# Kernel tuning notes

Measured on AMD Instinct MI355X. Metric: run time of the kernel, lower is better.

Reference implementation:

```python
import jax, jax.numpy as jnp
import numpy as np

EPS = 1e-7
BURN_IN = 3
INNER_STEPS = 2
N_FEAT, N_TARGET, N_LATENT = 262144, 8192, 32


def setup_inputs() -> dict:
    key = jax.random.key(0)
    ks = jax.random.split(key, 8)
    x = jax.random.normal(ks[0], (N_FEAT,), jnp.float32)
    y = jax.random.normal(ks[1], (N_TARGET,), jnp.float32)
    mu_x = jnp.zeros((N_FEAT,), jnp.float32)
    mu_y = jnp.zeros((N_TARGET,), jnp.float32)
    u0 = jax.random.normal(ks[2], (N_LATENT,), jnp.float32)
    u = u0 / jnp.sqrt(jnp.sum(u0 ** 2))
    Wz = jax.random.normal(ks[3], (N_LATENT, N_FEAT), jnp.float32) * 0.1
    Cz = jax.random.normal(ks[4], (N_LATENT, N_TARGET), jnp.float32) * 0.1
    t_sq_sum = jax.random.uniform(ks[5], (N_LATENT,), jnp.float32) + 1.0
    bz = jax.random.normal(ks[6], (N_LATENT,), jnp.float32) * 0.1
    P = jax.random.normal(ks[7], (N_LATENT, N_FEAT), jnp.float32) * 0.1
    return dict(x=x, y=y, mu_x=mu_x, mu_y=mu_y, u=u, Wz=Wz, Cz=Cz,
                t_sq_sum=t_sq_sum, bz=bz, P=P, n=100)


def _partial_fit(x, y, mu_x, mu_y, u, Wz, Cz, t_sq_sum, bz, P, n):
    # n is a static Python int (sample count before this call)
    n_new = n + 1  # torch: self.n[:] = self.n + 1
    mu_x = (mu_x * n_new + x) / (n_new + 1)
    mu_y = (mu_y * n_new + y) / (n_new + 1)
    xc = x - mu_x
    yc = y - mu_y
    if n_new <= BURN_IN:
        # vectorized burn-in update; only Wz and t_sq_sum change
        Wz = Wz + xc[None, :] * u[:, None]
        tz = Wz @ xc / (jnp.sqrt(jnp.sum(Wz ** 2, axis=1)) + EPS)
        t_sq_sum = t_sq_sum + tz * tz
        return mu_x, mu_y, u, Wz, Cz, t_sq_sum, bz, P

    def comp_step(carry, comp):
        xr, yr = carry
        Wz_i, Cz_i, P_i, u_i, tss, bz_i = comp
        # inner power-iteration refinements (total INNER_STEPS passes)
        for _ in range(INNER_STEPS):
            wz = Wz_i + xr * u_i                                  # [n_feat]
            tz = xr @ wz / (jnp.sqrt(jnp.sum(wz ** 2)) + EPS)     # scalar
            tss_ = tss + tz * tz
            t = tz / jnp.sqrt(tss_)
            cz = Cz_i + yr * t                                    # [n_target]
            C_i = cz / jnp.sqrt(jnp.sum(cz ** 2))
            u_i = yr @ C_i
        bz_new = bz_i + u_i * tz
        b = bz_new / jnp.sqrt(tss_)
        P_new = P_i + xr * t
        xr2 = xr - t * P_new  # deflate x
        yr2 = yr - b * t * C_i  # deflate y
        return (xr2, yr2), (wz, cz, P_new, u_i, tss_, bz_new)

    (_, _), (Wz_n, Cz_n, P_n, u_n, tss_n, bz_n) = jax.lax.scan(
        comp_step, (xc, yc), (Wz, Cz, P, u, t_sq_sum, bz))
    return mu_x, mu_y, u_n, Wz_n, Cz_n, tss_n, bz_n, P_n


def reference(x, y, mu_x, mu_y, u, Wz, Cz, t_sq_sum, bz, P, n):
    outs = _partial_fit(x, y, mu_x, mu_y, u, Wz, Cz, t_sq_sum, bz, P, n)
    # concatenate updated state (mu_x, mu_y, u, Wz, Cz, t_sq_sum, bz, P)
    return jnp.concatenate([o.ravel() for o in outs])
```

## Files before the change

kernel.cpp:

```cpp
#include <hip/hip_runtime.h>


#define NF 262144
#define NT 8192
#define NL 32
#define GYS 36
#define LDSW 260

#define NBX 1024
#define KS  256
#define CHK 128
#define NCHK 2
#define NSLOT 128
#define GXW 68
#define PBE 2276
#define DIAG 2244

#define WS_PART 0
#define WS_GY   (NSLOT*PBE)
#define WS_GX   (WS_GY + GYS*GYS)
#define WS_COEF (WS_GX + PBE)

#define OUT_MU_X 0
#define OUT_MU_Y 262144
#define OUT_U    270336
#define OUT_WZ   270368
#define OUT_CZ   8658976
#define OUT_TSS  8921120
#define OUT_BZ   8921152
#define OUT_P    8921184

typedef __attribute__((ext_vector_type(8))) short bf16x8;
typedef __attribute__((ext_vector_type(4))) float f32x4;

__device__ __forceinline__ float4 ld4(const float* p) { return *(const float4*)p; }

__device__ __forceinline__ unsigned int f2bf_rne(float f) {
  unsigned int t = __float_as_uint(f);
  t += 0x7FFFu + ((t >> 16) & 1u);
  return t >> 16;
}

__device__ __forceinline__ double rsq64(double x) {
  double r = __builtin_amdgcn_rsq(x);
  r = r * (1.5 - 0.5 * x * r * r);
  return r;
}

__global__ __launch_bounds__(320) void gram_kernel(
    const float* __restrict__ x, const float* __restrict__ y,
    const float* __restrict__ mux, const float* __restrict__ muy,
    const float* __restrict__ Wz, const float* __restrict__ Cz,
    const float* __restrict__ P, const int* __restrict__ np,
    float* __restrict__ ws)
{
  __shared__ __align__(16) char smem[80 * CHK * 4 + 128];
  const int tid = threadIdx.x;
  const int b = blockIdx.x;
  const float n1 = (float)(np[0] + 1);
  const float cmu = n1 / (n1 + 1.0f);

  if (b < NBX) {
    char* hB = smem;
    char* lB = smem + 80 * CHK * 2;
    float* PB = ws + WS_PART + (size_t)(b & (NSLOT - 1)) * PBE;

    {
      unsigned int* hz = (unsigned int*)hB;
      unsigned int* lz = (unsigned int*)lB;
      for (int i = tid; i < 960; i += 320) { hz[65 * 64 + i] = 0u; lz[65 * 64 + i] = 0u; }
    }

    f32x4 acc0 = {0.f, 0.f, 0.f, 0.f};
    f32x4 acc1 = acc0, acc2 = acc0;
    const int lane = tid & 63;
    const int w = tid >> 6;
    const int col16 = lane & 15;
    const int kgrp = lane >> 4;
    const int swz = (col16 & 7) << 4;

    float4 vA[7], vB[7]; float4 vmA, vmB;

    auto issue = [&](int c, float4* v, float4& vm) {
      const int kb = b * KS + c * CHK;
#pragma unroll
      for (int it = 0; it < 7; ++it) {
        int idx = tid + it * 320;
        if (idx < 2080) {
          int row = idx >> 5;
          int c4 = idx & 31;
          int k = kb + c4 * 4;
          const float* bp = (row == 0) ? (x + k)
                          : (row < 33) ? (P + (size_t)(row - 1) * NF + k)
                                       : (Wz + (size_t)(row - 33) * NF + k);
          v[it] = ld4(bp);
          if (it == 0 && row == 0) vm = ld4(mux + k);
        }
      }
    };

    auto convert_write = [&](float4* v, float4& vm) {
#pragma unroll
      for (int it = 0; it < 7; ++it) {
        int idx = tid + it * 320;
        if (idx < 2080) {
          int row = idx >> 5;
          int c4 = idx & 31;
          float4 t4 = v[it];
          if (it == 0 && row == 0) {
            t4.x = cmu * (t4.x - vm.x); t4.y = cmu * (t4.y - vm.y);
            t4.z = cmu * (t4.z - vm.z); t4.w = cmu * (t4.w - vm.w);
          }
          if (row >= 33) {
            float sq = t4.x * t4.x + t4.y * t4.y + t4.z * t4.z + t4.w * t4.w;
            sq += __shfl_xor(sq, 1, 64);
            sq += __shfl_xor(sq, 2, 64);
            sq += __shfl_xor(sq, 4, 64);
            sq += __shfl_xor(sq, 8, 64);
            sq += __shfl_xor(sq, 16, 64);
            if ((tid & 31) == 0) atomicAdd(&PB[DIAG + row - 33], sq);
          }
          unsigned int b0 = __float_as_uint(t4.x), b1 = __float_as_uint(t4.y);
          unsigned int b2 = __float_as_uint(t4.z), b3 = __float_as_uint(t4.w);
          float h0 = __uint_as_float(b0 & 0xFFFF0000u);
          float h1 = __uint_as_float(b1 & 0xFFFF0000u);
          float h2 = __uint_as_float(b2 & 0xFFFF0000u);
          float h3 = __uint_as_float(b3 & 0xFFFF0000u);
          uint2 hw, lw;
          hw.x = (b0 >> 16) | ((b1 >> 16) << 16);
          hw.y = (b2 >> 16) | ((b3 >> 16) << 16);
          lw.x = f2bf_rne(t4.x - h0) | (f2bf_rne(t4.y - h1) << 16);
          lw.y = f2bf_rne(t4.z - h2) | (f2bf_rne(t4.w - h3) << 16);
          int off = ((row << 8) + (c4 << 3)) ^ ((row & 7) << 4);
          *(uint2*)(hB + off) = hw;
          *(uint2*)(lB + off) = lw;
        }
      }
    };

    auto compute_chunk = [&]() {
#pragma unroll
      for (int s = 0; s < 4; ++s) {
        const int kbyte = s * 64 + kgrp * 16;
        const int oa = ((col16 << 8) + kbyte) ^ swz;
        const int ob = oa + (w << 12);
        bf16x8 bh = *(const bf16x8*)(hB + ob);
        bf16x8 bl = *(const bf16x8*)(lB + ob);
        bf16x8 a0h = *(const bf16x8*)(hB + oa);
        bf16x8 a0l = *(const bf16x8*)(lB + oa);
        acc0 = __builtin_amdgcn_mfma_f32_16x16x32_bf16(a0h, bh, acc0, 0, 0, 0);
        acc0 = __builtin_amdgcn_mfma_f32_16x16x32_bf16(a0h, bl, acc0, 0, 0, 0);
        acc0 = __builtin_amdgcn_mfma_f32_16x16x32_bf16(a0l, bh, acc0, 0, 0, 0);
        acc0 = __builtin_amdgcn_mfma_f32_16x16x32_bf16(a0l, bl, acc0, 0, 0, 0);
        bf16x8 a1h = *(const bf16x8*)(hB + oa + 4096);
        bf16x8 a1l = *(const bf16x8*)(lB + oa + 4096);
        acc1 = __builtin_amdgcn_mfma_f32_16x16x32_bf16(a1h, bh, acc1, 0, 0, 0);
        acc1 = __builtin_amdgcn_mfma_f32_16x16x32_bf16(a1h, bl, acc1, 0, 0, 0);
        acc1 = __builtin_amdgcn_mfma_f32_16x16x32_bf16(a1l, bh, acc1, 0, 0, 0);
        acc1 = __builtin_amdgcn_mfma_f32_16x16x32_bf16(a1l, bl, acc1, 0, 0, 0);
        bf16x8 a2h = *(const bf16x8*)(hB + oa + 8192);
        bf16x8 a2l = *(const bf16x8*)(lB + oa + 8192);
        acc2 = __builtin_amdgcn_mfma_f32_16x16x32_bf16(a2h, bh, acc2, 0, 0, 0);
        acc2 = __builtin_amdgcn_mfma_f32_16x16x32_bf16(a2h, bl, acc2, 0, 0, 0);
        acc2 = __builtin_amdgcn_mfma_f32_16x16x32_bf16(a2l, bh, acc2, 0, 0, 0);
        acc2 = __builtin_amdgcn_mfma_f32_16x16x32_bf16(a2l, bl, acc2, 0, 0, 0);
      }
    };

    issue(0, vA, vmA);
    issue(1, vB, vmB);
    convert_write(vA, vmA);
    __syncthreads();
    compute_chunk();
    __syncthreads();
    convert_write(vB, vmB);
    __syncthreads();
    compute_chunk();

    const int vcol = w * 16 + col16;
    if (vcol < 65) {
#pragma unroll
      for (int r2 = 0; r2 < 4; ++r2) {
        int u = kgrp * 4 + r2;
        atomicAdd(&PB[u * GXW + vcol], acc0[r2]);
        atomicAdd(&PB[(16 + u) * GXW + vcol], acc1[r2]);
      }
      if (kgrp == 0) atomicAdd(&PB[32 * GXW + vcol], acc2[0]);
    }
  } else {
    float* lds = (float*)smem;
    float* GY = ws + WS_GY;
    const int yb = b - NBX;
    int gu = 0, gv = 0; bool active = (tid < 45);
    if (active) {
      int pp = tid;
      for (int g = 0; g < 9; ++g) {
        int cnt = 9 - g;
        if (pp < cnt) { gu = g; gv = g + pp; break; }
        pp -= cnt;
      }
    }
    float acc[16];
#pragma unroll
    for (int i = 0; i < 16; ++i) acc[i] = 0.f;
    const int wb = yb * 256;
    float4 vy[8]; float4 vmy;
#pragma unroll
    for (int it = 0; it < 8; ++it) {
      int idx = tid + it * 320;
      if (idx < 2304) {
        int row = idx >> 6;
        int c4 = idx & 63;
        int k = wb + c4 * 4;
        if (row == 0) {
          vy[it] = ld4(y + k);
          if (it == 0) vmy = ld4(muy + k);
        } else if (row < 33) {
          vy[it] = ld4(Cz + (size_t)(row - 1) * NT + k);
        } else {
          vy[it] = make_float4(0.f, 0.f, 0.f, 0.f);
        }
      }
    }
#pragma unroll
    for (int it = 0; it < 8; ++it) {
      int idx = tid + it * 320;
      if (idx < 2304) {
        int row = idx >> 6;
        int c4 = idx & 63;
        float4 t4 = vy[it];
        if (it == 0 && row == 0) {
          t4.x = cmu * (t4.x - vmy.x); t4.y = cmu * (t4.y - vmy.y);
          t4.z = cmu * (t4.z - vmy.z); t4.w = cmu * (t4.w - vmy.w);
        }
        *(float4*)&lds[row * LDSW + c4 * 4] = t4;
      }
    }
    __syncthreads();
    if (active) {
      const int ub = 4 * gu * LDSW, vb = 4 * gv * LDSW;
      for (int c = 0; c < 64; ++c) {
        float4 av[4], bv[4];
#pragma unroll
        for (int r = 0; r < 4; ++r) av[r] = *(const float4*)&lds[ub + r * LDSW + c * 4];
#pragma unroll
        for (int s = 0; s < 4; ++s) bv[s] = *(const float4*)&lds[vb + s * LDSW + c * 4];
#pragma unroll
        for (int r = 0; r < 4; ++r)
#pragma unroll
          for (int s = 0; s < 4; ++s)
            acc[r * 4 + s] += av[r].x * bv[s].x + av[r].y * bv[s].y +
                              av[r].z * bv[s].z + av[r].w * bv[s].w;
      }
#pragma unroll
      for (int r = 0; r < 4; ++r)
#pragma unroll
        for (int s = 0; s < 4; ++s) {
          int u = 4 * gu + r, v = 4 * gv + s;
          if (u < 33 && v < 33) {
            float val = acc[r * 4 + s];
            atomicAdd(&GY[u * GYS + v], val);
            if (gu != gv) atomicAdd(&GY[v * GYS + u], val);
          }
        }
    }
  }
}

__global__ __launch_bounds__(256) void reduce_kernel(float* __restrict__ ws) {
  const int e = (blockIdx.x % 9) * 256 + threadIdx.x;
  const int c = blockIdx.x / 9;
  if (e < PBE) {
    const float* PB = ws + WS_PART + (size_t)(c * 32) * PBE + e;
    float s0 = 0.f, s1 = 0.f, s2 = 0.f, s3 = 0.f;
#pragma unroll
    for (int j = 0; j < 32; j += 4) {
      s0 += PB[(size_t)j * PBE];
      s1 += PB[(size_t)(j + 1) * PBE];
      s2 += PB[(size_t)(j + 2) * PBE];
      s3 += PB[(size_t)(j + 3) * PBE];
    }
    atomicAdd(ws + WS_GX + e, (s0 + s1) + (s2 + s3));
  }
}

__global__ void solve_kernel(const float* __restrict__ ws,
                             const float* __restrict__ u_in,
                             const float* __restrict__ tss_in,
                             const float* __restrict__ bz_in,
                             float* __restrict__ coef,
                             float* __restrict__ out)
{
  const int l = threadIdx.x;
  const float* GX = ws + WS_GX;
  const float* GY = ws + WS_GY;
  float* AWZT = coef;
  float* APT  = coef + 33 * NL;
  float* ACZT = coef + 66 * NL;

  float rP[32], rW[32], rC[32];
#pragma unroll
  for (int i = 0; i < 32; ++i) rP[i] = GX[(1 + i) * GXW + 1 + l];
#pragma unroll
  for (int i = 0; i < 32; ++i) rW[i] = (l < 32) ? GX[(1 + i) * GXW + 33 + l] : 0.f;
#pragma unroll
  for (int i = 0; i < 32; ++i) rC[i] = GY[(1 + i) * GYS + 1 + l];
  float dS  = (l < 32) ? GX[DIAG + l] : 0.f;
  float u0l = (l < 32) ? u_in[l]   : 0.f;
  float t0l = (l < 32) ? tss_in[l] : 0.f;
  float b0l = (l < 32) ? bz_in[l]  : 0.f;

  double q = (double)GX[0];
  double r = (double)GY[0];
  double pj = (l < 32) ? (double)GX[1 + l]  : 0.0;
  double wj = (l < 32) ? (double)GX[33 + l] : 0.0;
  double ej = (l < 32) ? (double)GY[1 + l]  : 0.0;
  double cx = (l == 0) ? 1.0 : 0.0;
  double cy = (l == 0) ? 1.0 : 0.0;

#pragma unroll
  for (int i = 0; i < NL; ++i) {
    double a  = __shfl(wj, i, 64);
    double g  = __shfl(ej, i, 64);
    double pi = __shfl(pj, i, 64);
    double s  = (double)__shfl(dS, i, 64);
    double h  = (double)__shfl(rC[i], i, 64);
    double Pd = (double)__shfl(rP[i], i, 64);
    double u0   = (double)__shfl(u0l, i, 64);
    double tss0 = (double)__shfl(t0l, i, 64);
    double bz0  = (double)__shfl(b0l, i, 64);

    double ui = u0, u1 = 0.0, tz = 0.0, tss_ = 0.0, t = 0.0;
    double rt = 0.0, rn = 0.0;
#pragma unroll
    for (int pass = 0; pass < 2; ++pass) {
      double num = a + ui * q;
      double s2  = s + 2.0 * ui * a + ui * ui * q;
      double rs  = rsq64(s2);
      tz = num * rs * (1.0 - 1e-7 * rs);
      tss_ = tss0 + tz * tz;
      rt = rsq64(tss_);
      t  = tz * rt;
      double ncz2 = h + 2.0 * t * g + t * t * r;
      rn = rsq64(ncz2);
      ui = (g + t * r) * rn;
      if (pass == 0) u1 = ui;
    }
    double u2 = ui;
    double bz_new = bz0 + u2 * tz;
    double bb = bz_new * rt;
    double phi = 1.0 - t * t;
    double gam = bb * t * rn;
    double psi = 1.0 - gam * t;

    if (l == 0) {
      out[OUT_U + i]   = (float)u2;
      out[OUT_TSS + i] = (float)tss_;
      out[OUT_BZ + i]  = (float)bz_new;
    }
    if (l < 33) {
      AWZT[l * 32 + i] = (float)(u1 * cx);
      APT [l * 32 + i] = (float)(t  * cx) + ((l == 1 + i) ? 1.0f : 0.0f);
      ACZT[l * 32 + i] = (float)(t  * cy) + ((l == 1 + i) ? 1.0f : 0.0f);
    }
    q = phi * phi * q - 2.0 * phi * t * pi + t * t * Pd;
    r = psi * psi * r - 2.0 * psi * gam * g + gam * gam * h;
    cx *= phi; if (l == 1 + i) cx -= t;
    cy *= psi; if (l == 1 + i) cy -= gam;
    if (l < 32) {
      pj = phi * pj - t * (double)rP[i];
      wj = phi * wj - t * (double)rW[i];
      ej = psi * ej - gam * (double)rC[i];
    }
  }
}

__global__ __launch_bounds__(256) void out_kernel(
    const float* __restrict__ x, const float* __restrict__ y,
    const float* __restrict__ mux, const float* __restrict__ muy,
    const float* __restrict__ Wz, const float* __restrict__ Cz,
    const float* __restrict__ P, const int* __restrict__ np,
    const float* __restrict__ coef, float* __restrict__ out)
{
  const int b = blockIdx.x, tid = threadIdx.x;
  const float n1 = (float)(np[0] + 1);
  const float inv = 1.0f / (n1 + 1.0f);
  const float* AWZT = coef;
  const float* APT  = coef + 33 * NL;
  const float* ACZT = coef + 66 * NL;

  if (b < 1024) {
    const int k = b * 256 + tid;
    float xv = x[k], mv = mux[k];
    float mn = (mv * n1 + xv) * inv;
    out[OUT_MU_X + k] = mn;
    float accW[32], accP[32];
#pragma unroll
    for (int i = 0; i < 32; ++i) accW[i] = Wz[(size_t)i * NF + k];
#pragma unroll
    for (int i = 0; i < 32; ++i) accP[i] = 0.f;
    {
      float B0 = xv - mn;
#pragma unroll
      for (int i = 0; i < 32; ++i) {
        accW[i] += AWZT[i] * B0;
        accP[i] += APT[i] * B0;
      }
    }
#pragma unroll 4
    for (int j = 1; j < 33; ++j) {
      float Bj = P[(size_t)(j - 1) * NF + k];
      const float* cw = AWZT + j * 32;
      const float* cp = APT + j * 32;
#pragma unroll
      for (int i = 0; i < 32; ++i) {
        accW[i] += cw[i] * Bj;
        accP[i] += cp[i] * Bj;
      }
    }
#pragma unroll
    for (int i = 0; i < 32; ++i) out[OUT_WZ + (size_t)i * NF + k] = accW[i];
#pragma unroll
    for (int i = 0; i < 32; ++i) out[OUT_P + (size_t)i * NF + k] = accP[i];
  } else {
    const int k = (b - 1024) * 256 + tid;
    float yv = y[k], mv = muy[k];
    float mn = (mv * n1 + yv) * inv;
    out[OUT_MU_Y + k] = mn;
    float accC[32];
#pragma unroll
    for (int i = 0; i < 32; ++i) accC[i] = 0.f;
    {
      float B0 = yv - mn;
#pragma unroll
      for (int i = 0; i < 32; ++i) accC[i] += ACZT[i] * B0;
    }
#pragma unroll 4
    for (int j = 1; j < 33; ++j) {
      float Bj = Cz[(size_t)(j - 1) * NT + k];
      const float* cc = ACZT + j * 32;
#pragma unroll
      for (int i = 0; i < 32; ++i) accC[i] += cc[i] * Bj;
    }
#pragma unroll
    for (int i = 0; i < 32; ++i) out[OUT_CZ + (size_t)i * NT + k] = accC[i];
  }
}

extern "C" void kernel_launch(void* const* d_in, const int* in_sizes, int n_in,
                              void* d_out, int out_size, void* d_ws, size_t ws_size,
                              hipStream_t stream) {
  const float* x   = (const float*)d_in[0];
  const float* y   = (const float*)d_in[1];
  const float* mux = (const float*)d_in[2];
  const float* muy = (const float*)d_in[3];
  const float* u   = (const float*)d_in[4];
  const float* Wz  = (const float*)d_in[5];
  const float* Cz  = (const float*)d_in[6];
  const float* tss = (const float*)d_in[7];
  const float* bz  = (const float*)d_in[8];
  const float* P   = (const float*)d_in[9];
  const int*   n   = (const int*)d_in[10];
  float* ws  = (float*)d_ws;
  float* out = (float*)d_out;

  hipMemsetAsync(ws, 0, (size_t)(NSLOT * PBE + GYS * GYS + PBE) * sizeof(float), stream);
  gram_kernel<<<NBX + 32, 320, 0, stream>>>(x, y, mux, muy, Wz, Cz, P, n, ws);
  reduce_kernel<<<36, 256, 0, stream>>>(ws);
  solve_kernel<<<1, 64, 0, stream>>>(ws, u, tss, bz, ws + WS_COEF, out);
  out_kernel<<<1024 + 32, 256, 0, stream>>>(x, y, mux, muy, Wz, Cz, P, n, ws + WS_COEF, out);
}
```

Measured before the change: 228.1 us.

## Fuse reduce and solve via last-block counter; widen partial slots; single-buffer gram loads

Merges the reduce and single-block solve kernels into one launch, where the last block to finish (found with an atomic counter) runs the solve, removing one kernel launch boundary. Partial-sum slots grow from 128 to 512 to cut atomic contention in the gram kernel, at the cost of a larger memset and more reduction traffic. The gram kernel drops its double register buffer and issues the second chunk's loads after the first barrier, lowering register pressure but exposing more load latency.

```diff
diff --git a/kernel.cpp b/kernel.cpp
--- a/kernel.cpp
+++ b/kernel.cpp
@@ -10,8 +10,7 @@
 #define NBX 1024
 #define KS  256
 #define CHK 128
-#define NCHK 2
-#define NSLOT 128
+#define NSLOT 512
 #define GXW 68
 #define PBE 2276
 #define DIAG 2244
@@ -19,7 +18,8 @@
 #define WS_PART 0
 #define WS_GY   (NSLOT*PBE)
 #define WS_GX   (WS_GY + GYS*GYS)
-#define WS_COEF (WS_GX + PBE)
+#define WS_CNT  (WS_GX + PBE)
+#define WS_COEF (WS_CNT + 4)
 
 #define OUT_MU_X 0
 #define OUT_MU_Y 262144
@@ -79,9 +79,9 @@
     const int kgrp = lane >> 4;
     const int swz = (col16 & 7) << 4;
 
-    float4 vA[7], vB[7]; float4 vmA, vmB;
-
-    auto issue = [&](int c, float4* v, float4& vm) {
+    float4 v[7]; float4 vm0;
+
+    auto issue = [&](int c) {
       const int kb = b * KS + c * CHK;
 #pragma unroll
       for (int it = 0; it < 7; ++it) {
@@ -94,12 +94,12 @@
                           : (row < 33) ? (P + (size_t)(row - 1) * NF + k)
                                        : (Wz + (size_t)(row - 33) * NF + k);
           v[it] = ld4(bp);
-          if (it == 0 && row == 0) vm = ld4(mux + k);
+          if (it == 0 && row == 0) vm0 = ld4(mux + k);
         }
       }
     };
 
-    auto convert_write = [&](float4* v, float4& vm) {
+    auto convert_write = [&]() {
 #pragma unroll
       for (int it = 0; it < 7; ++it) {
         int idx = tid + it * 320;
@@ -108,8 +108,8 @@
           int c4 = idx & 31;
           float4 t4 = v[it];
           if (it == 0 && row == 0) {
-            t4.x = cmu * (t4.x - vm.x); t4.y = cmu * (t4.y - vm.y);
-            t4.z = cmu * (t4.z - vm.z); t4.w = cmu * (t4.w - vm.w);
+            t4.x = cmu * (t4.x - vm0.x); t4.y = cmu * (t4.y - vm0.y);
+            t4.z = cmu * (t4.z - vm0.z); t4.w = cmu * (t4.w - vm0.w);
           }
           if (row >= 33) {
             float sq = t4.x * t4.x + t4.y * t4.y + t4.z * t4.z + t4.w * t4.w;
@@ -167,13 +167,13 @@
       }
     };
 
-    issue(0, vA, vmA);
-    issue(1, vB, vmB);
-    convert_write(vA, vmA);
+    issue(0);
+    convert_write();
     __syncthreads();
+    issue(1);
     compute_chunk();
     __syncthreads();
-    convert_write(vB, vmB);
+    convert_write();
     __syncthreads();
     compute_chunk();
 
@@ -267,29 +267,10 @@
   }
 }
 
-__global__ __launch_bounds__(256) void reduce_kernel(float* __restrict__ ws) {
-  const int e = (blockIdx.x % 9) * 256 + threadIdx.x;
-  const int c = blockIdx.x / 9;
-  if (e < PBE) {
-    const float* PB = ws + WS_PART + (size_t)(c * 32) * PBE + e;
-    float s0 = 0.f, s1 = 0.f, s2 = 0.f, s3 = 0.f;
-#pragma unroll
-    for (int j = 0; j < 32; j += 4) {
-      s0 += PB[(size_t)j * PBE];
-      s1 += PB[(size_t)(j + 1) * PBE];
-      s2 += PB[(size_t)(j + 2) * PBE];
-      s3 += PB[(size_t)(j + 3) * PBE];
-    }
-    atomicAdd(ws + WS_GX + e, (s0 + s1) + (s2 + s3));
-  }
-}
-
-__global__ void solve_kernel(const float* __restrict__ ws,
-                             const float* __restrict__ u_in,
-                             const float* __restrict__ tss_in,
-                             const float* __restrict__ bz_in,
-                             float* __restrict__ coef,
-                             float* __restrict__ out)
+__device__ __forceinline__ void solve_body(
+    const float* __restrict__ ws, const float* __restrict__ u_in,
+    const float* __restrict__ tss_in, const float* __restrict__ bz_in,
+    float* __restrict__ coef, float* __restrict__ out)
 {
   const int l = threadIdx.x;
   const float* GX = ws + WS_GX;
@@ -373,6 +354,37 @@
       ej = psi * ej - gam * (double)rC[i];
     }
   }
+}
+
+__global__ __launch_bounds__(256) void redsolve_kernel(
+    float* __restrict__ ws, const float* __restrict__ u_in,
+    const float* __restrict__ tss_in, const float* __restrict__ bz_in,
+    float* __restrict__ coef, float* __restrict__ out)
+{
+  const int e = (blockIdx.x % 9) * 256 + threadIdx.x;
+  const int c = blockIdx.x / 9;
+  if (e < PBE) {
+    const float* PB = ws + WS_PART + (size_t)(c * 64) * PBE + e;
+    float s0 = 0.f, s1 = 0.f, s2 = 0.f, s3 = 0.f;
+#pragma unroll
+    for (int j = 0; j < 64; j += 4) {
+      s0 += PB[(size_t)j * PBE];
+      s1 += PB[(size_t)(j + 1) * PBE];
+      s2 += PB[(size_t)(j + 2) * PBE];
+      s3 += PB[(size_t)(j + 3) * PBE];
+    }
+    atomicAdd(ws + WS_GX + e, (s0 + s1) + (s2 + s3));
+  }
+  __threadfence();
+  __shared__ int lastflag;
+  if (threadIdx.x == 0) {
+    int old = atomicAdd((int*)(ws + WS_CNT), 1);
+    lastflag = (old == 71);
+  }
+  __syncthreads();
+  if (!lastflag) return;
+  __threadfence();
+  if (threadIdx.x < 64) solve_body(ws, u_in, tss_in, bz_in, coef, out);
 }
 
 __global__ __launch_bounds__(256) void out_kernel(
@@ -464,9 +476,8 @@
   float* ws  = (float*)d_ws;
   float* out = (float*)d_out;
 
-  hipMemsetAsync(ws, 0, (size_t)(NSLOT * PBE + GYS * GYS + PBE) * sizeof(float), stream);
+  hipMemsetAsync(ws, 0, (size_t)(NSLOT * PBE + GYS * GYS + PBE + 4) * sizeof(float), stream);
   gram_kernel<<<NBX + 32, 320, 0, stream>>>(x, y, mux, muy, Wz, Cz, P, n, ws);
-  reduce_kernel<<<36, 256, 0, stream>>>(ws);
-  solve_kernel<<<1, 64, 0, stream>>>(ws, u, tss, bz, ws + WS_COEF, out);
+  redsolve_kernel<<<72, 256, 0, stream>>>(ws, u, tss, bz, ws + WS_COEF, out);
   out_kernel<<<1024 + 32, 256, 0, stream>>>(x, y, mux, muy, Wz, Cz, P, n, ws + WS_COEF, out);
 }
```

Result: faster. 220.4 us (-3.4%).
